# Performance work log

Measured on AMD Instinct MI355X. Metric: run time of the kernel, lower is better.

## Reference

```python
import jax, jax.numpy as jnp
import numpy as np

ALPHA_IT = 0.7   # GraphLearner.alpha_it
BETA_IT = 0.5    # GraphLearner.beta_it
B = 4            # hardcoded expand(4, -1, -1) => class_num must be 4
EPS = 1e-12      # F.normalize eps


def _edge_emb(x):
    # x: [B, K, n]; L2-normalize over feature dim K, then Gram matrix over nodes
    xn = x / jnp.clip(jnp.linalg.norm(x, axis=1, keepdims=True), EPS)
    return jnp.einsum('bkn,bkm->bnm', xn, xn)  # [B, n, n]


def _gcn(feat, adj, W, b):
    # feat: [B, K, n], adj: [B, n, n], W: [K, K], b: [B, K]
    n = adj.shape[1]
    adj = jnp.clip(adj, 0.0) + jnp.eye(n, dtype=adj.dtype)[None]
    d = adj.sum(-1)                                   # [B, n]
    dinv = jnp.where(d > 0, d ** -0.5, 0.0)           # inf -> 0 as in torch
    # D A D expressed as row/col scaling (equivalent to the dense diag bmm)
    norm_adj = dinv[:, :, None] * adj * dinv[:, None, :]
    x = feat.transpose(0, 2, 1)                        # [B, n, K]
    pre = x @ W                                        # [B, n, K]
    out = norm_adj @ pre + b[:, None, :]               # [B, n, K]
    return jnp.tanh(out[:, 0, :])                      # [B, K]


def setup_inputs() -> dict:
    key = jax.random.key(0)
    ks = jax.random.split(key, 7)
    C, D = 4, 512
    stdv = 1.0 / np.sqrt(D)
    return {
        'base_text_features': jax.random.normal(ks[0], (C, D), dtype=jnp.float32),
        'base_img_features': jax.random.normal(ks[1], (C, D), dtype=jnp.float32),
        'img_feature': jax.random.normal(ks[2], (40960, D), dtype=jnp.float32),
        'W_tt': jax.random.uniform(ks[3], (D, D), minval=-stdv, maxval=stdv, dtype=jnp.float32),
        'b_tt': jnp.zeros((C, D), dtype=jnp.float32),
        'W_it': jax.random.uniform(ks[4], (D, D), minval=-stdv, maxval=stdv, dtype=jnp.float32),
        'b_it': jnp.zeros((C, D), dtype=jnp.float32),
    }


def reference(base_text_features, base_img_features, img_feature, W_tt, b_tt, W_it, b_it):
    # torch computes feats/edges under no_grad + detach
    bt = jax.lax.stop_gradient(base_text_features)
    bi = jax.lax.stop_gradient(base_img_features)
    D = bt.shape[1]
    inputs_text = bt[:, None, :]                              # [4, 1, D]
    node_tt = jnp.broadcast_to(bt[None], (B, B, D))           # [4, 4, D]
    node_it = jnp.broadcast_to(bi[None], (B, B, D))
    feat_tt = jnp.concatenate([inputs_text, node_tt], axis=1).transpose(0, 2, 1)  # [4, D, 5]
    feat_it = jnp.concatenate([inputs_text, node_it], axis=1).transpose(0, 2, 1)
    edge_tt = _edge_emb(feat_tt)                              # [4, 5, 5]
    edge_it = _edge_emb(feat_it)
    g_tt = _gcn(feat_tt, edge_tt, W_tt, b_tt)                 # [4, D]
    g_it = _gcn(feat_it, edge_it, W_it, b_it)
    graph_o_t = ALPHA_IT * g_tt + (1.0 - ALPHA_IT) * g_it
    refined = BETA_IT * base_text_features + (1.0 - BETA_IT) * graph_o_t
    return (refined, img_feature)
```

## Files before the change

kernel.cpp:

```cpp
#include <hip/hip_runtime.h>

#define DD 512
#define NMM 16
#define COLS 32
#define SLICES 16
#define NCOPY 2048
#define EPSF 1e-12f

typedef float f32x4 __attribute__((ext_vector_type(4)));

__global__ __launch_bounds__(512) void graph_fused(
    const float* __restrict__ bt,
    const float* __restrict__ bi,
    const float* __restrict__ img,
    const float* __restrict__ Wtt,
    const float* __restrict__ btt,
    const float* __restrict__ Wit,
    const float* __restrict__ bit_,
    float* __restrict__ out)
{
    const int bid = blockIdx.x;
    const int tid = threadIdx.x;

    if (bid >= NMM) {
        const f32x4* __restrict__ src = (const f32x4*)img;
        f32x4* __restrict__ dst = (f32x4*)(out + 4 * DD);
        const long long t = (long long)(bid - NMM) * 512 + tid;
        const long long S = (long long)NCOPY * 512;
        f32x4 v0 = src[t + 0 * S];
        f32x4 v1 = src[t + 1 * S];
        f32x4 v2 = src[t + 2 * S];
        f32x4 v3 = src[t + 3 * S];
        f32x4 v4 = src[t + 4 * S];
        dst[t + 0 * S] = v0;
        dst[t + 1 * S] = v1;
        dst[t + 2 * S] = v2;
        dst[t + 3 * S] = v3;
        dst[t + 4 * S] = v4;
        return;
    }

    __shared__ float dots[36];
    __shared__ float coef[4][9];
    __shared__ float u[2][4][DD];
    __shared__ float red[8][SLICES][COLS];

    {
        const int pi_[10] = {0,0,0,0,1,1,1,2,2,3};
        const int pj_[10] = {0,1,2,3,1,2,3,2,3,3};
        const int wave = tid >> 6;
        const int lane = tid & 63;
        for (int dotid = wave; dotid < 36; dotid += 8) {
            const float *uu, *vv;
            if (dotid < 10)      { uu = bt + pi_[dotid] * DD;      vv = bt + pj_[dotid] * DD; }
            else if (dotid < 20) { uu = bi + pi_[dotid - 10] * DD; vv = bi + pj_[dotid - 10] * DD; }
            else { int r = dotid - 20; uu = bt + (r >> 2) * DD;    vv = bi + (r & 3) * DD; }
            float s = 0.f;
            #pragma unroll
            for (int e = lane; e < DD; e += 64) s += uu[e] * vv[e];
            #pragma unroll
            for (int off = 32; off; off >>= 1) s += __shfl_xor(s, off, 64);
            if (lane == 0) dots[dotid] = s;
        }
    }
    __syncthreads();

    if (tid < 4) {
        const int b = tid;
        auto pidx = [](int i, int j) -> int {
            if (i > j) { int t = i; i = j; j = t; }
            const int base[4] = {0, 4, 7, 9};
            return base[i] + (j - i);
        };
        float ntn[4], nin[4];
        #pragma unroll
        for (int i = 0; i < 4; i++) ntn[i] = fmaxf(sqrtf(dots[pidx(i, i)]), EPSF);
        #pragma unroll
        for (int i = 0; i < 4; i++) nin[i] = fmaxf(sqrtf(dots[10 + pidx(i, i)]), EPSF);

        {
            int map[5] = {b, 0, 1, 2, 3};
            float adj[5][5];
            #pragma unroll
            for (int r = 0; r < 5; r++)
                #pragma unroll
                for (int c = 0; c < 5; c++) {
                    float cv = dots[pidx(map[r], map[c])] / (ntn[map[r]] * ntn[map[c]]);
                    adj[r][c] = fmaxf(cv, 0.f) + (r == c ? 1.f : 0.f);
                }
            float dinv[5];
            #pragma unroll
            for (int r = 0; r < 5; r++) {
                float dd = 0.f;
                #pragma unroll
                for (int c = 0; c < 5; c++) dd += adj[r][c];
                dinv[r] = 1.0f / sqrtf(dd);
            }
            float w[5];
            #pragma unroll
            for (int j = 0; j < 5; j++) w[j] = dinv[0] * adj[0][j] * dinv[j];
            float ct[4] = {w[1], w[2], w[3], w[4]};
            ct[b] += w[0];
            #pragma unroll
            for (int i = 0; i < 4; i++) coef[b][i] = ct[i];
        }
        {
            float adj[5][5];
            #pragma unroll
            for (int r = 0; r < 5; r++)
                #pragma unroll
                for (int c = 0; c < 5; c++) {
                    float cv;
                    if (r == 0 && c == 0)      cv = dots[pidx(b, b)] / (ntn[b] * ntn[b]);
                    else if (r == 0)           cv = dots[20 + b * 4 + (c - 1)] / (ntn[b] * nin[c - 1]);
                    else if (c == 0)           cv = dots[20 + b * 4 + (r - 1)] / (ntn[b] * nin[r - 1]);
                    else                       cv = dots[10 + pidx(r - 1, c - 1)] / (nin[r - 1] * nin[c - 1]);
                    adj[r][c] = fmaxf(cv, 0.f) + (r == c ? 1.f : 0.f);
                }
            float dinv[5];
            #pragma unroll
            for (int r = 0; r < 5; r++) {
                float dd = 0.f;
                #pragma unroll
                for (int c = 0; c < 5; c++) dd += adj[r][c];
                dinv[r] = 1.0f / sqrtf(dd);
            }
            float w[5];
            #pragma unroll
            for (int j = 0; j < 5; j++) w[j] = dinv[0] * adj[0][j] * dinv[j];
            coef[b][4] = w[0];
            #pragma unroll
            for (int j = 0; j < 4; j++) coef[b][5 + j] = w[j + 1];
        }
    }
    __syncthreads();

    {
        const int k = tid;
        #pragma unroll
        for (int b = 0; b < 4; b++) {
            float s1 = 0.f;
            #pragma unroll
            for (int i = 0; i < 4; i++) s1 += coef[b][i] * bt[i * DD + k];
            u[0][b][k] = s1;
            float s2 = coef[b][4] * bt[b * DD + k];
            #pragma unroll
            for (int j = 0; j < 4; j++) s2 += coef[b][5 + j] * bi[j * DD + k];
            u[1][b][k] = s2;
        }
    }
    __syncthreads();

    {
        const int c  = tid & (COLS - 1);
        const int ks = tid >> 5;
        const int col = bid * COLS + c;
        const int k0 = ks * (DD / SLICES);
        float acc[2][4] = {};
        const float* __restrict__ Ws[2] = {Wtt, Wit};
        #pragma unroll
        for (int m = 0; m < 2; m++) {
            const float* __restrict__ W = Ws[m];
            #pragma unroll 8
            for (int kk = 0; kk < DD / SLICES; kk++) {
                const int k = k0 + kk;
                const float w = W[k * DD + col];
                #pragma unroll
                for (int b = 0; b < 4; b++) acc[m][b] += u[m][b][k] * w;
            }
        }
        #pragma unroll
        for (int m = 0; m < 2; m++)
            #pragma unroll
            for (int b = 0; b < 4; b++)
                red[m * 4 + b][ks][c] = acc[m][b];
    }
    __syncthreads();

    if (tid < 4 * COLS) {
        const int c = tid & (COLS - 1);
        const int b = tid >> 5;
        const int col = bid * COLS + c;
        float stt = 0.f, sit = 0.f;
        #pragma unroll
        for (int s = 0; s < SLICES; s++) {
            stt += red[b][s][c];
            sit += red[4 + b][s][c];
        }
        const float g_tt = tanhf(stt + btt[b * DD + col]);
        const float g_it = tanhf(sit + bit_[b * DD + col]);
        const float go   = 0.7f * g_tt + 0.3f * g_it;
        out[b * DD + col] = 0.5f * bt[b * DD + col] + 0.5f * go;
    }
}

extern "C" void kernel_launch(void* const* d_in, const int* in_sizes, int n_in,
                              void* d_out, int out_size, void* d_ws, size_t ws_size,
                              hipStream_t stream) {
    const float* bt   = (const float*)d_in[0];
    const float* bi   = (const float*)d_in[1];
    const float* img  = (const float*)d_in[2];
    const float* Wtt  = (const float*)d_in[3];
    const float* btt  = (const float*)d_in[4];
    const float* Wit  = (const float*)d_in[5];
    const float* bit_ = (const float*)d_in[6];
    float* out = (float*)d_out;

    graph_fused<<<NMM + NCOPY, 512, 0, stream>>>(bt, bi, img, Wtt, btt, Wit, bit_, out);
}
```

Baseline: 169.0 us.

## Split image copy into separate kernel with nontemporal stores and deeper per-thread loads

Moves the large img_feature passthrough copy out of the fused kernel into its own kernel of 256-thread blocks. Each thread now loads 10 vectors before storing them, and the stores are nontemporal. The small graph computation runs as a second 16-block launch. The aim is more memory-level parallelism and less cache pollution on the bandwidth-bound copy. The cost is an extra kernel launch and the loss of overlap between the graph blocks and the copy.

```diff
diff --git a/kernel.cpp b/kernel.cpp
--- a/kernel.cpp
+++ b/kernel.cpp
@@ -4,15 +4,27 @@
 #define NMM 16
 #define COLS 32
 #define SLICES 16
-#define NCOPY 2048
 #define EPSF 1e-12f
 
 typedef float f32x4 __attribute__((ext_vector_type(4)));
 
-__global__ __launch_bounds__(512) void graph_fused(
+__global__ __launch_bounds__(256) void copy_kernel(
+    const float* __restrict__ img, float* __restrict__ out)
+{
+    const f32x4* __restrict__ src = (const f32x4*)img;
+    f32x4* __restrict__ dst = (f32x4*)(out + 4 * DD);
+    const long long S = 2048LL * 256;
+    const long long t = (long long)blockIdx.x * 256 + threadIdx.x;
+    f32x4 v[10];
+    #pragma unroll
+    for (int j = 0; j < 10; j++) v[j] = src[t + j * S];
+    #pragma unroll
+    for (int j = 0; j < 10; j++) __builtin_nontemporal_store(v[j], &dst[t + j * S]);
+}
+
+__global__ __launch_bounds__(512) void graph_kernel(
     const float* __restrict__ bt,
     const float* __restrict__ bi,
-    const float* __restrict__ img,
     const float* __restrict__ Wtt,
     const float* __restrict__ btt,
     const float* __restrict__ Wit,
@@ -21,24 +33,6 @@
 {
     const int bid = blockIdx.x;
     const int tid = threadIdx.x;
-
-    if (bid >= NMM) {
-        const f32x4* __restrict__ src = (const f32x4*)img;
-        f32x4* __restrict__ dst = (f32x4*)(out + 4 * DD);
-        const long long t = (long long)(bid - NMM) * 512 + tid;
-        const long long S = (long long)NCOPY * 512;
-        f32x4 v0 = src[t + 0 * S];
-        f32x4 v1 = src[t + 1 * S];
-        f32x4 v2 = src[t + 2 * S];
-        f32x4 v3 = src[t + 3 * S];
-        f32x4 v4 = src[t + 4 * S];
-        dst[t + 0 * S] = v0;
-        dst[t + 1 * S] = v1;
-        dst[t + 2 * S] = v2;
-        dst[t + 3 * S] = v3;
-        dst[t + 4 * S] = v4;
-        return;
-    }
 
     __shared__ float dots[36];
     __shared__ float coef[4][9];
@@ -206,5 +200,6 @@
     const float* bit_ = (const float*)d_in[6];
     float* out = (float*)d_out;
 
-    graph_fused<<<NMM + NCOPY, 512, 0, stream>>>(bt, bi, img, Wtt, btt, Wit, bit_, out);
+    copy_kernel<<<2048, 256, 0, stream>>>(img, out);
+    graph_kernel<<<NMM, 512, 0, stream>>>(bt, bi, Wtt, btt, Wit, bit_, out);
 }
```

After: 185.3 us. 9.7% more time.
